# Kernel tuning notes

Hardware: AMD Instinct MI355X
Metric: run time of the kernel (lower is better)

Reference implementation:

```python
import jax, jax.numpy as jnp
import numpy as np

N = 100000   # nodes
E = 1600000  # edges (before self-loops)
HIDDEN = 256
BN_EPS = 1e-5


def setup_inputs() -> dict:
    key = jax.random.key(0)
    ks = jax.random.split(key, 16)
    def lin(k, i, o):
        return jax.random.normal(k, (i, o), jnp.float32) / np.float32(np.sqrt(i))
    inp = {
        "x": jax.random.normal(ks[0], (N, 21), jnp.float32),
        "edge_index": jax.random.randint(ks[1], (2, E), 0, N),
        # GCNConv weights (stored [in, out]) + biases
        "W1": lin(ks[2], 21, HIDDEN), "b1": jnp.zeros((HIDDEN,), jnp.float32),
        "W2": lin(ks[3], HIDDEN, 112), "b2": jnp.zeros((112,), jnp.float32),
        # dense MLP
        "lin2_w": lin(ks[4], 112, 256), "lin2_b": jnp.zeros((256,), jnp.float32),
        "lin3_w": lin(ks[5], 256, 100), "lin3_b": jnp.zeros((100,), jnp.float32),
        "lin4_w": lin(ks[6], 100, 1),   "lin4_b": jnp.zeros((1,), jnp.float32),
        # batchnorm affine params
        "g1": jnp.ones((112,), jnp.float32), "be1": jnp.zeros((112,), jnp.float32),
        "g2": jnp.ones((256,), jnp.float32), "be2": jnp.zeros((256,), jnp.float32),
        "g3": jnp.ones((100,), jnp.float32), "be3": jnp.zeros((100,), jnp.float32),
    }
    return inp


def _gcn_conv(x, W, b, src, dst, n):
    # PyG GCNConv: h = xW; out_i = sum_j norm_ij * h_j (+ bias), sym-normalized w/ self-loops
    h = x @ W                                              # [N, C]
    deg = jax.ops.segment_sum(jnp.ones(src.shape, h.dtype), dst, num_segments=n)
    dinv = jnp.where(deg > 0, jax.lax.rsqrt(deg), 0.0)
    norm = dinv[src] * dinv[dst]                            # [E']
    out = jax.ops.segment_sum(h[src] * norm[:, None], dst, num_segments=n)
    return out + b


def _bn(x, g, b):
    # train-mode batchnorm: biased batch variance
    m = jnp.mean(x, axis=0)
    v = jnp.mean(jnp.square(x - m), axis=0)
    return (x - m) * jax.lax.rsqrt(v + BN_EPS) * g + b


def reference(x, edge_index, W1, b1, W2, b2, lin2_w, lin2_b, lin3_w, lin3_b,
              lin4_w, lin4_b, g1, be1, g2, be2, g3, be3):
    n = x.shape[0]
    loops = jnp.arange(n, dtype=edge_index.dtype)
    src = jnp.concatenate([edge_index[0], loops])
    dst = jnp.concatenate([edge_index[1], loops])
    h = jax.nn.relu(_gcn_conv(x, W1, b1, src, dst, n))
    h = _gcn_conv(h, W2, b2, src, dst, n)
    h = jax.nn.relu(_bn(h, g1, be1))
    # dropout: identity (eval / deterministic)
    h = jax.nn.relu(_bn(h @ lin2_w + lin2_b, g2, be2))
    h = jax.nn.relu(_bn(h @ lin3_w + lin3_b, g3, be3))
    return h @ lin4_w + lin4_b
```

## Files before the change

kernel.cpp:

```cpp
#include <hip/hip_runtime.h>

#define N_NODES 100000
#define N_EDGES 1600000

typedef _Float16 f16x8 __attribute__((ext_vector_type(8)));
typedef _Float16 f16x4 __attribute__((ext_vector_type(4)));
typedef float fx4 __attribute__((ext_vector_type(4)));

#define NREP 16
#define NBUCK 196
#define CHUNK 8192
#define BCAP 12288

__global__ __launch_bounds__(256) void k_bin(const int* __restrict__ ei,
                                             unsigned* __restrict__ binned,
                                             int* __restrict__ gcount) {
  __shared__ unsigned pr[CHUNK];
  __shared__ unsigned srt[CHUNK];
  __shared__ unsigned char bk[CHUNK];
  __shared__ int hist[256], scanb[256], offs[256], bs[256], gb[256];
  const int t = threadIdx.x;
  const int e0 = blockIdx.x * CHUNK;
  const int n = min(CHUNK, N_EDGES - e0);
  hist[t] = 0;
  __syncthreads();
  for (int i = t; i < n; i += 256) {
    int src = ei[e0 + i], dst = ei[N_EDGES + e0 + i];
    int b = dst >> 9;
    pr[i] = ((unsigned)src << 9) | (unsigned)(dst & 511);
    bk[i] = (unsigned char)b;
    atomicAdd(&hist[b], 1);
  }
  __syncthreads();
  int v = hist[t];
  scanb[t] = v;
  __syncthreads();
  for (int off = 1; off < 256; off <<= 1) {
    int a = (t >= off) ? scanb[t - off] : 0;
    __syncthreads();
    scanb[t] += a;
    __syncthreads();
  }
  offs[t] = scanb[t] - v;
  bs[t] = scanb[t] - v;
  __syncthreads();
  for (int i = t; i < n; i += 256) {
    int b = bk[i];
    int p = atomicAdd(&offs[b], 1);
    srt[p] = pr[i];
  }
  if (t < NBUCK && v > 0) gb[t] = atomicAdd(&gcount[t], v);
  __syncthreads();
  int wave = t >> 6, lane = t & 63;
  for (int b = wave; b < NBUCK; b += 4) {
    int c = hist[b];
    if (c == 0) continue;
    int ls = bs[b], base = gb[b];
    unsigned* dstp = binned + (size_t)b * BCAP + base;
    for (int i = lane; i < c; i += 64) dstp[i] = srt[ls + i];
  }
}

__global__ void k_bscan(const int* __restrict__ gcount, int* __restrict__ gbase) {
  __shared__ int s[256];
  int t = threadIdx.x;
  int v = (t < NBUCK) ? gcount[t] : 0;
  s[t] = v;
  __syncthreads();
  for (int off = 1; off < 256; off <<= 1) {
    int a = (t >= off) ? s[t - off] : 0;
    __syncthreads();
    s[t] += a;
    __syncthreads();
  }
  if (t < NBUCK) gbase[t] = s[t] - v;
}

__global__ __launch_bounds__(256) void k_csr(const unsigned* __restrict__ binned,
                                             const int* __restrict__ gcount,
                                             const int* __restrict__ gbase,
                                             int* __restrict__ rowoff,
                                             int* __restrict__ cnt,
                                             float* __restrict__ dinv,
                                             int* __restrict__ csr) {
  __shared__ int hist[512], offs[512], ps[256];
  __shared__ unsigned srt[BCAP];
  const int b = blockIdx.x, t = threadIdx.x;
  const int n = min(gcount[b], BCAP);
  const int gb0 = gbase[b];
  const unsigned* bp = binned + (size_t)b * BCAP;
  hist[t] = 0;
  hist[t + 256] = 0;
  __syncthreads();
  for (int i = t; i < n; i += 256) atomicAdd(&hist[bp[i] & 511], 1);
  __syncthreads();
  int e0v = hist[2 * t], e1v = hist[2 * t + 1];
  ps[t] = e0v + e1v;
  __syncthreads();
  for (int off = 1; off < 256; off <<= 1) {
    int a = (t >= off) ? ps[t - off] : 0;
    __syncthreads();
    ps[t] += a;
    __syncthreads();
  }
  int excl = ps[t] - (e0v + e1v);
  offs[2 * t] = excl;
  offs[2 * t + 1] = excl + e0v;
  __syncthreads();
#pragma unroll
  for (int u = 0; u < 2; ++u) {
    int j = 2 * t + u;
    int nd = (b << 9) + j;
    if (nd < N_NODES) {
      int c = hist[j];
      cnt[nd] = c;
      dinv[nd] = rsqrtf((float)(c + 1));
      rowoff[nd] = gb0 + offs[j];
    }
  }
  __syncthreads();
  for (int i = t; i < n; i += 256) {
    unsigned p = bp[i];
    int d = p & 511;
    int pos = atomicAdd(&offs[d], 1);
    srt[pos] = p >> 9;
  }
  __syncthreads();
  for (int i = t; i < n; i += 256) csr[gb0 + i] = (int)srt[i];
}

__global__ void k_xpad(const float* __restrict__ x, const float* __restrict__ dinv,
                       _Float16* __restrict__ xs) {
  int idx = blockIdx.x * 256 + threadIdx.x;
  if (idx >= N_NODES * 24) return;
  int r = idx / 24, c = idx - r * 24;
  xs[idx] = (_Float16)((c < 21) ? x[r * 21 + c] * dinv[r] : 0.f);
}

__global__ __launch_bounds__(256) void k_aggx(
    const f16x8* __restrict__ xs3, const float* __restrict__ dinv,
    const int* __restrict__ rowoff, const int* __restrict__ cnt,
    const int* __restrict__ csr, float* __restrict__ aggx) {
  int lane = threadIdx.x & 63, wave = threadIdx.x >> 6;
  int j = lane / 3, c = lane - j * 3;
  if (j >= 21) return;
  int i = blockIdx.x * 84 + wave * 21 + j;
  if (i >= N_NODES) return;
  float di = dinv[i];
  int start = rowoff[i], len = cnt[i];
  f16x8 u = xs3[i * 3 + c];
  float a0[8], a1[8], a2[8], a3[8];
#pragma unroll
  for (int t = 0; t < 8; ++t) { a0[t] = (float)u[t]; a1[t] = a2[t] = a3[t] = 0.f; }
  int e = 0;
  for (; e + 3 < len; e += 4) {
    int s0 = csr[start + e], s1 = csr[start + e + 1];
    int s2 = csr[start + e + 2], s3 = csr[start + e + 3];
    f16x8 u0 = xs3[s0 * 3 + c];
    f16x8 u1 = xs3[s1 * 3 + c];
    f16x8 u2 = xs3[s2 * 3 + c];
    f16x8 u3 = xs3[s3 * 3 + c];
#pragma unroll
    for (int t = 0; t < 8; ++t) {
      a0[t] += (float)u0[t]; a1[t] += (float)u1[t];
      a2[t] += (float)u2[t]; a3[t] += (float)u3[t];
    }
  }
  for (; e < len; ++e) {
    int s0 = csr[start + e];
    f16x8 u0 = xs3[s0 * 3 + c];
#pragma unroll
    for (int t = 0; t < 8; ++t) a0[t] += (float)u0[t];
  }
  float4 r0, r1;
  r0.x = di * (a0[0] + a1[0] + a2[0] + a3[0]);
  r0.y = di * (a0[1] + a1[1] + a2[1] + a3[1]);
  r0.z = di * (a0[2] + a1[2] + a2[2] + a3[2]);
  r0.w = di * (a0[3] + a1[3] + a2[3] + a3[3]);
  r1.x = di * (a0[4] + a1[4] + a2[4] + a3[4]);
  r1.y = di * (a0[5] + a1[5] + a2[5] + a3[5]);
  r1.z = di * (a0[6] + a1[6] + a2[6] + a3[6]);
  r1.w = di * (a0[7] + a1[7] + a2[7] + a3[7]);
  *(float4*)(aggx + (size_t)i * 24 + c * 8) = r0;
  *(float4*)(aggx + (size_t)i * 24 + c * 8 + 4) = r1;
}

__global__ __launch_bounds__(256) void k_gemm1(const float4* __restrict__ aggx4,
                                               const float* __restrict__ W1,
                                               const float* __restrict__ b1,
                                               _Float16* __restrict__ h1) {
  __shared__ float As[32][24];
  int t = threadIdx.x;
  int base = blockIdx.x * 32;
  for (int idx = t; idx < 32 * 6; idx += 256) {
    int m = idx / 6, q = idx - m * 6;
    *(float4*)(&As[m][q * 4]) = aggx4[(base + m) * 6 + q];
  }
  float w[21];
#pragma unroll
  for (int k = 0; k < 21; ++k) w[k] = W1[k * 256 + t];
  float bias = b1[t];
  __syncthreads();
  for (int m = 0; m < 32; ++m) {
    float acc = bias;
#pragma unroll
    for (int k = 0; k < 21; ++k) acc = fmaf(As[m][k], w[k], acc);
    h1[(size_t)(base + m) * 256 + t] = (_Float16)fmaxf(acc, 0.f);
  }
}

template <int K, int KPAD, int NOUT, int NR>
__global__ void k_wcvt(const float* __restrict__ W, _Float16* __restrict__ Wh) {
  int idx = blockIdx.x * 256 + threadIdx.x;
  if (idx >= NR * KPAD) return;
  int n = idx / KPAD, k = idx % KPAD;
  float v = (n < NOUT && k < K) ? W[k * NOUT + n] : 0.f;
  Wh[idx] = (_Float16)v;
}

template <int K, int KPAD, int NT, int MT, int WR, int WC, int MINW,
          bool BN, bool STATS, bool F16IN, bool F16OUT, bool SPLIT>
__global__ __launch_bounds__(256, MINW) void k_mgemm(
    const void* __restrict__ Av, const _Float16* __restrict__ Wt,
    const float* __restrict__ bias, const float* __restrict__ bn_a,
    const float* __restrict__ bn_c, const float* __restrict__ rowscale,
    void* __restrict__ Cv, void* __restrict__ Cv2, int NOUTr,
    float* __restrict__ sums, float* __restrict__ sqs) {
  constexpr int BM = WR * MT * 16;
  constexpr int NR = WC * NT * 16;
  constexpr int BKP = 40;
  constexpr int NC = KPAD / 32;
  constexpr int AIT = BM * 4 / 256;
  constexpr int ABYTES = BM * BKP * 2;
  constexpr int BBYTES = NR * BKP * 2;
  __shared__ __align__(16) char smem[ABYTES + BBYTES];
  _Float16* Ah = (_Float16*)smem;
  _Float16* Bh = (_Float16*)(smem + ABYTES);
  const float* A32 = (const float*)Av;
  const _Float16* A16 = (const _Float16*)Av;
  float* C = (float*)Cv;
  _Float16* C16 = (_Float16*)Cv;
  _Float16* C16b = (_Float16*)Cv2;

  const int tid = threadIdx.x;
  const int lane = tid & 63, wave = tid >> 6;
  const int wr = wave % WR, wc = wave / WR;
  const int quad = lane >> 4, ln = lane & 15;
  const int rowbase = blockIdx.x * BM;

  fx4 acc[MT][NT];
#pragma unroll
  for (int mt = 0; mt < MT; ++mt)
#pragma unroll
    for (int j = 0; j < NT; ++j) acc[mt][j] = (fx4){0.f, 0.f, 0.f, 0.f};

  f16x8 pf16[AIT];
  fx4 pf32a[AIT], pf32b[AIT];

  auto loadA = [&](int kc) {
#pragma unroll
    for (int it = 0; it < AIT; ++it) {
      int idx = tid + it * 256;
      int m = idx >> 2, q = idx & 3;
      int gi = rowbase + m;
      int k = kc * 32 + q * 8;
      bool ok = (gi < N_NODES) && (k < K);
      if constexpr (F16IN) {
        f16x8 z;
#pragma unroll
        for (int t = 0; t < 8; ++t) z[t] = (_Float16)0;
        pf16[it] = ok ? *(const f16x8*)(A16 + (size_t)gi * K + k) : z;
      } else {
        if (ok) {
          pf32a[it] = *(const fx4*)(A32 + (size_t)gi * K + k);
          pf32b[it] = *(const fx4*)(A32 + (size_t)gi * K + k + 4);
        } else {
          pf32a[it] = (fx4){0.f, 0.f, 0.f, 0.f};
          pf32b[it] = (fx4){0.f, 0.f, 0.f, 0.f};
        }
      }
    }
  };

  auto writeA = [&](int kc) {
#pragma unroll
    for (int it = 0; it < AIT; ++it) {
      int idx = tid + it * 256;
      int m = idx >> 2, q = idx & 3;
      int k = kc * 32 + q * 8;
      float vv[8];
      if constexpr (F16IN) {
#pragma unroll
        for (int t = 0; t < 8; ++t) vv[t] = (float)pf16[it][t];
      } else {
#pragma unroll
        for (int t = 0; t < 4; ++t) { vv[t] = pf32a[it][t]; vv[t + 4] = pf32b[it][t]; }
      }
      if constexpr (BN) {
        if (k < K) {
          float4 a0 = *(const float4*)(bn_a + k);
          float4 a1 = *(const float4*)(bn_a + k + 4);
          float4 c0 = *(const float4*)(bn_c + k);
          float4 c1 = *(const float4*)(bn_c + k + 4);
          float av[8] = {a0.x, a0.y, a0.z, a0.w, a1.x, a1.y, a1.z, a1.w};
          float cv[8] = {c0.x, c0.y, c0.z, c0.w, c1.x, c1.y, c1.z, c1.w};
#pragma unroll
          for (int t = 0; t < 8; ++t) vv[t] = fmaxf(fmaf(vv[t], av[t], cv[t]), 0.f);
        }
      }
      f16x8 hv;
#pragma unroll
      for (int t = 0; t < 8; ++t) hv[t] = (_Float16)vv[t];
      *(f16x8*)(Ah + m * BKP + q * 8) = hv;
    }
  };

  loadA(0);
  for (int kc = 0; kc < NC; ++kc) {
    __syncthreads();
    writeA(kc);
    for (int idx = tid; idx < NR * 4; idx += 256) {
      int n = idx >> 2, p = idx & 3;
      *(f16x8*)(Bh + n * BKP + p * 8) =
          *(const f16x8*)(Wt + n * KPAD + kc * 32 + p * 8);
    }
    __syncthreads();
    if (kc + 1 < NC) loadA(kc + 1);
    f16x8 nf[MT];
#pragma unroll
    for (int mt = 0; mt < MT; ++mt) {
      int r = (wr * MT + mt) * 16 + ln;
      nf[mt] = *(const f16x8*)(Ah + r * BKP + quad * 8);
    }
#pragma unroll
    for (int j = 0; j < NT; ++j) {
      int n = (wc * NT + j) * 16 + ln;
      f16x8 wh = *(const f16x8*)(Bh + n * BKP + quad * 8);
#pragma unroll
      for (int mt = 0; mt < MT; ++mt)
        acc[mt][j] = __builtin_amdgcn_mfma_f32_16x16x32_f16(wh, nf[mt], acc[mt][j], 0, 0, 0);
    }
  }

  float* s_s = (float*)smem;
  float* s_q = s_s + NR;
  __syncthreads();
  if constexpr (STATS) {
    for (int c = tid; c < 2 * NR; c += 256) s_s[c] = 0.f;
    __syncthreads();
  }
  float rs[MT];
#pragma unroll
  for (int mt = 0; mt < MT; ++mt) {
    int nd = rowbase + (wr * MT + mt) * 16 + ln;
    rs[mt] = (rowscale != nullptr && nd < N_NODES) ? rowscale[nd] : 1.f;
  }
#pragma unroll
  for (int j = 0; j < NT; ++j) {
    int ch0 = (wc * NT + j) * 16 + quad * 4;
    bool cv = ch0 < NOUTr;
    float4 b4 = make_float4(0.f, 0.f, 0.f, 0.f);
    if (cv && bias != nullptr) b4 = *(const float4*)(bias + ch0);
    float sc[4] = {0.f, 0.f, 0.f, 0.f}, sq[4] = {0.f, 0.f, 0.f, 0.f};
#pragma unroll
    for (int mt = 0; mt < MT; ++mt) {
      int nd = rowbase + (wr * MT + mt) * 16 + ln;
      if (nd < N_NODES && cv) {
        float v0 = (acc[mt][j][0] + b4.x) * rs[mt];
        float v1 = (acc[mt][j][1] + b4.y) * rs[mt];
        float v2 = (acc[mt][j][2] + b4.z) * rs[mt];
        float v3 = (acc[mt][j][3] + b4.w) * rs[mt];
        if constexpr (F16OUT) {
          f16x4 o = {(_Float16)v0, (_Float16)v1, (_Float16)v2, (_Float16)v3};
          if constexpr (SPLIT) {
            _Float16* dp = (ch0 < 56)
                ? C16 + (size_t)nd * 64 + ch0
                : C16b + (size_t)nd * 64 + (ch0 - 56);
            *(f16x4*)dp = o;
          } else {
            *(f16x4*)(C16 + (size_t)nd * NOUTr + ch0) = o;
          }
        } else {
          float4 o = make_float4(v0, v1, v2, v3);
          *(float4*)(C + (size_t)nd * NOUTr + ch0) = o;
        }
        if constexpr (STATS) {
          sc[0] += v0; sq[0] = fmaf(v0, v0, sq[0]);
          sc[1] += v1; sq[1] = fmaf(v1, v1, sq[1]);
          sc[2] += v2; sq[2] = fmaf(v2, v2, sq[2]);
          sc[3] += v3; sq[3] = fmaf(v3, v3, sq[3]);
        }
      }
    }
    if constexpr (STATS) {
      if (cv) {
#pragma unroll
        for (int r = 0; r < 4; ++r) {
          float s = sc[r], q = sq[r];
          s += __shfl_xor(s, 1); q += __shfl_xor(q, 1);
          s += __shfl_xor(s, 2); q += __shfl_xor(q, 2);
          s += __shfl_xor(s, 4); q += __shfl_xor(q, 4);
          s += __shfl_xor(s, 8); q += __shfl_xor(q, 8);
          if (ln == 0) {
            atomicAdd(&s_s[ch0 + r], s);
            atomicAdd(&s_q[ch0 + r], q);
          }
        }
      }
    }
  }
  if constexpr (STATS) {
    __syncthreads();
    int rep = (blockIdx.x & (NREP - 1));
    for (int c = tid; c < NR; c += 256) {
      if (c < NOUTr) {
        atomicAdd(&sums[rep * NOUTr + c], s_s[c]);
        atomicAdd(&sqs[rep * NOUTr + c], s_q[c]);
      }
    }
  }
}

__global__ __launch_bounds__(256) void k_agg2(
    const f16x8* __restrict__ t2x8, const float* __restrict__ dinv,
    const int* __restrict__ rowoff, const int* __restrict__ cnt,
    const int* __restrict__ csr, const float* __restrict__ b2,
    _Float16* __restrict__ g2, int off) {
  int lane = threadIdx.x & 63, wave = threadIdx.x >> 6;
  int j = lane >> 3, c = lane & 7;
  int i = blockIdx.x * 32 + wave * 8 + j;
  float di = dinv[i];
  int start = rowoff[i], len = cnt[i];
  f16x8 u = t2x8[i * 8 + c];
  float a0[8], a1[8], a2[8], a3[8];
#pragma unroll
  for (int t = 0; t < 8; ++t) { a0[t] = (float)u[t]; a1[t] = a2[t] = a3[t] = 0.f; }
  int e = 0;
  for (; e + 3 < len; e += 4) {
    int s0 = csr[start + e], s1 = csr[start + e + 1];
    int s2 = csr[start + e + 2], s3 = csr[start + e + 3];
    f16x8 u0 = t2x8[s0 * 8 + c];
    f16x8 u1 = t2x8[s1 * 8 + c];
    f16x8 u2 = t2x8[s2 * 8 + c];
    f16x8 u3 = t2x8[s3 * 8 + c];
#pragma unroll
    for (int t = 0; t < 8; ++t) {
      a0[t] += (float)u0[t]; a1[t] += (float)u1[t];
      a2[t] += (float)u2[t]; a3[t] += (float)u3[t];
    }
  }
  for (; e < len; ++e) {
    int s0 = csr[start + e];
    f16x8 u0 = t2x8[s0 * 8 + c];
#pragma unroll
    for (int t = 0; t < 8; ++t) a0[t] += (float)u0[t];
  }
  if (c < 7) {
    float4 blo = *(const float4*)(b2 + off + c * 8);
    float4 bhi = *(const float4*)(b2 + off + c * 8 + 4);
    float bb[8] = {blo.x, blo.y, blo.z, blo.w, bhi.x, bhi.y, bhi.z, bhi.w};
    f16x8 o;
#pragma unroll
    for (int t = 0; t < 8; ++t)
      o[t] = (_Float16)fmaf(di, a0[t] + a1[t] + a2[t] + a3[t], bb[t]);
    *(f16x8*)(g2 + (size_t)i * 112 + off + c * 8) = o;
  }
}

template <int C>
__global__ void k_colstats16(const _Float16* __restrict__ X, float* __restrict__ sums,
                             float* __restrict__ sqs) {
  int c = threadIdx.x;
  if (c >= C) return;
  int chunk = (N_NODES + gridDim.x - 1) / gridDim.x;
  int i0 = blockIdx.x * chunk;
  int i1 = min(N_NODES, i0 + chunk);
  float s = 0.f, q = 0.f;
  for (int i = i0; i < i1; ++i) {
    float v = (float)X[(size_t)i * C + c];
    s += v;
    q = fmaf(v, v, q);
  }
  int rep = (blockIdx.x & (NREP - 1));
  atomicAdd(&sums[rep * C + c], s);
  atomicAdd(&sqs[rep * C + c], q);
}

template <int C>
__global__ void k_bnfinal(const float* __restrict__ sums, const float* __restrict__ sqs,
                          const float* __restrict__ gamma, const float* __restrict__ beta,
                          float* __restrict__ bn_a, float* __restrict__ bn_c) {
  int c = threadIdx.x;
  if (c >= C) return;
  float s = 0.f, q = 0.f;
#pragma unroll
  for (int r = 0; r < NREP; ++r) {
    s += sums[r * C + c];
    q += sqs[r * C + c];
  }
  const float inv_n = 1.0f / (float)N_NODES;
  float mean = s * inv_n;
  float var = fmaxf(q * inv_n - mean * mean, 0.f);
  float rstd = 1.0f / sqrtf(var + 1e-5f);
  float a = gamma[c] * rstd;
  bn_a[c] = a;
  bn_c[c] = beta[c] - mean * a;
}

__global__ void k_final(const float* __restrict__ h4, const float* __restrict__ bn_a,
                        const float* __restrict__ bn_c, const float* __restrict__ w4,
                        const float* __restrict__ b4, float* __restrict__ out) {
  int lane = threadIdx.x & 63;
  int i = blockIdx.x * 4 + (threadIdx.x >> 6);
  float acc = fmaxf(fmaf(h4[(size_t)i * 100 + lane], bn_a[lane], bn_c[lane]), 0.f) * w4[lane];
  if (lane < 36) {
    int k = lane + 64;
    acc += fmaxf(fmaf(h4[(size_t)i * 100 + k], bn_a[k], bn_c[k]), 0.f) * w4[k];
  }
#pragma unroll
  for (int off = 32; off >= 1; off >>= 1) acc += __shfl_down(acc, off);
  if (lane == 0) out[i] = acc + b4[0];
}

extern "C" void kernel_launch(void* const* d_in, const int* in_sizes, int n_in,
                              void* d_out, int out_size, void* d_ws, size_t ws_size,
                              hipStream_t stream) {
  const float* x   = (const float*)d_in[0];
  const int*   ei  = (const int*)d_in[1];
  const float* W1  = (const float*)d_in[2];
  const float* b1  = (const float*)d_in[3];
  const float* W2  = (const float*)d_in[4];
  const float* b2  = (const float*)d_in[5];
  const float* l2w = (const float*)d_in[6];
  const float* l2b = (const float*)d_in[7];
  const float* l3w = (const float*)d_in[8];
  const float* l3b = (const float*)d_in[9];
  const float* l4w = (const float*)d_in[10];
  const float* l4b = (const float*)d_in[11];
  const float* g1  = (const float*)d_in[12];
  const float* be1 = (const float*)d_in[13];
  const float* g2w = (const float*)d_in[14];
  const float* be2 = (const float*)d_in[15];
  const float* g3  = (const float*)d_in[16];
  const float* be3 = (const float*)d_in[17];
  float* out = (float*)d_out;

  char* base = (char*)d_ws;
  size_t off = 0;
  auto alloc = [&](size_t bytes) -> char* {
    char* p = base + off;
    off = (off + bytes + 255) & ~(size_t)255;
    return p;
  };
  int*   cnt    = (int*)alloc((size_t)N_NODES * 4);
  int*   rowoff = (int*)alloc((size_t)N_NODES * 4);
  float* dinv   = (float*)alloc((size_t)N_NODES * 4);
  int*   csr    = (int*)alloc((size_t)N_EDGES * 4);
  unsigned* binned = (unsigned*)alloc((size_t)NBUCK * BCAP * 4);
  int*   gcount = (int*)alloc(NBUCK * 4);
  int*   gbase  = (int*)alloc(NBUCK * 4);
  float* stats  = (float*)alloc((size_t)NREP * 960 * 4);
  float* bnco   = (float*)alloc(960 * 4);
  _Float16* xs  = (_Float16*)alloc((size_t)N_NODES * 24 * 2);
  float* aggx   = (float*)alloc((size_t)N_NODES * 24 * 4);
  _Float16* h1  = (_Float16*)alloc((size_t)N_NODES * 256 * 2);
  _Float16* t2a = (_Float16*)alloc((size_t)N_NODES * 64 * 2);
  _Float16* t2b = (_Float16*)alloc((size_t)N_NODES * 64 * 2);
  _Float16* g2h = (_Float16*)alloc((size_t)N_NODES * 112 * 2);
  float* h4     = (float*)alloc((size_t)N_NODES * 112 * 4);
  _Float16* wt2 = (_Float16*)alloc(112 * 256 * 2);
  _Float16* wt3 = (_Float16*)alloc(256 * 128 * 2);
  _Float16* wt4 = (_Float16*)alloc(112 * 256 * 2);

  float* sums1 = stats;
  float* sqs1  = sums1 + NREP * 112;
  float* sums2 = sqs1 + NREP * 112;
  float* sqs2  = sums2 + NREP * 256;
  float* sums3 = sqs2 + NREP * 256;
  float* sqs3  = sums3 + NREP * 112;
  float* bn_a1 = bnco + 0,   *bn_c1 = bnco + 112;
  float* bn_a2 = bnco + 224, *bn_c2 = bnco + 480;
  float* bn_a3 = bnco + 736, *bn_c3 = bnco + 848;

  hipMemsetAsync(gcount, 0, NBUCK * 4, stream);
  hipMemsetAsync(stats, 0, (size_t)NREP * 960 * 4, stream);

  k_bin<<<NBUCK, 256, 0, stream>>>(ei, binned, gcount);
  k_bscan<<<1, 256, 0, stream>>>(gcount, gbase);
  k_csr<<<NBUCK, 256, 0, stream>>>(binned, gcount, gbase, rowoff, cnt, dinv, csr);

  k_wcvt<256, 256, 112, 112><<<112, 256, 0, stream>>>(W2, wt2);
  k_wcvt<112, 128, 256, 256><<<128, 256, 0, stream>>>(l2w, wt3);
  k_wcvt<256, 256, 100, 112><<<112, 256, 0, stream>>>(l3w, wt4);

  k_xpad<<<(N_NODES * 24 + 255) / 256, 256, 0, stream>>>(x, dinv, xs);
  k_aggx<<<(N_NODES + 83) / 84, 256, 0, stream>>>((const f16x8*)xs, dinv, rowoff,
                                                  cnt, csr, aggx);
  k_gemm1<<<3125, 256, 0, stream>>>((const float4*)aggx, W1, b1, h1);

  k_mgemm<256, 256, 7, 2, 4, 1, 4, false, false, true, true, true>
      <<<782, 256, 0, stream>>>(h1, wt2, nullptr, nullptr, nullptr, dinv,
                                t2a, t2b, 112, nullptr, nullptr);
  k_agg2<<<3125, 256, 0, stream>>>((const f16x8*)t2a, dinv, rowoff, cnt, csr, b2,
                                   g2h, 0);
  k_agg2<<<3125, 256, 0, stream>>>((const f16x8*)t2b, dinv, rowoff, cnt, csr, b2,
                                   g2h, 56);

  k_colstats16<112><<<1600, 128, 0, stream>>>(g2h, sums1, sqs1);
  k_bnfinal<112><<<1, 128, 0, stream>>>(sums1, sqs1, g1, be1, bn_a1, bn_c1);

  k_mgemm<112, 128, 8, 2, 2, 2, 4, true, true, true, true, false>
      <<<1563, 256, 0, stream>>>(g2h, wt3, l2b, bn_a1, bn_c1, nullptr,
                                 h1, nullptr, 256, sums2, sqs2);
  k_bnfinal<256><<<1, 256, 0, stream>>>(sums2, sqs2, g2w, be2, bn_a2, bn_c2);

  k_mgemm<256, 256, 7, 2, 4, 1, 4, true, true, true, false, false>
      <<<782, 256, 0, stream>>>(h1, wt4, l3b, bn_a2, bn_c2, nullptr,
                                h4, nullptr, 100, sums3, sqs3);
  k_bnfinal<100><<<1, 128, 0, stream>>>(sums3, sqs3, g3, be3, bn_a3, bn_c3);

  k_final<<<25000, 256, 0, stream>>>(h4, bn_a3, bn_c3, l4w, l4b, out);
}
```

Baseline: 411.4 us.

## Restructure dense GEMM to preload full weight tile and load A directly to registers

The MFMA GEMM kernel now loads the whole weight tile (all K) into shared memory once and has each wave read its A fragments directly from global memory into registers. This removes the per-K-chunk A staging through LDS and the two barriers per iteration. The 256-wide GEMM is split across a second grid dimension over output channels, and the lin3 output buffer h4 is stored as fp16 instead of fp32 to halve its write and read traffic. The trade-off is that A loads are no longer software-prefetched, the B tile uses more shared memory, occupancy hints change, and h4 loses precision.

```diff
diff --git a/kernel.cpp b/kernel.cpp
--- a/kernel.cpp
+++ b/kernel.cpp
@@ -218,153 +218,103 @@
   Wh[idx] = (_Float16)v;
 }
 
-template <int K, int KPAD, int NT, int MT, int WR, int WC, int MINW,
-          bool BN, bool STATS, bool F16IN, bool F16OUT, bool SPLIT>
+template <int K, int KPAD, int NT, int MT, int MINW,
+          bool BN, bool STATS, bool F16OUT, bool SPLIT>
 __global__ __launch_bounds__(256, MINW) void k_mgemm(
-    const void* __restrict__ Av, const _Float16* __restrict__ Wt,
+    const _Float16* __restrict__ A16, const _Float16* __restrict__ Wt,
     const float* __restrict__ bias, const float* __restrict__ bn_a,
     const float* __restrict__ bn_c, const float* __restrict__ rowscale,
     void* __restrict__ Cv, void* __restrict__ Cv2, int NOUTr,
     float* __restrict__ sums, float* __restrict__ sqs) {
+  constexpr int WR = 4;
   constexpr int BM = WR * MT * 16;
-  constexpr int NR = WC * NT * 16;
-  constexpr int BKP = 40;
+  constexpr int NR = NT * 16;
+  constexpr int KPS = KPAD + 8;
   constexpr int NC = KPAD / 32;
-  constexpr int AIT = BM * 4 / 256;
-  constexpr int ABYTES = BM * BKP * 2;
-  constexpr int BBYTES = NR * BKP * 2;
-  __shared__ __align__(16) char smem[ABYTES + BBYTES];
-  _Float16* Ah = (_Float16*)smem;
-  _Float16* Bh = (_Float16*)(smem + ABYTES);
-  const float* A32 = (const float*)Av;
-  const _Float16* A16 = (const _Float16*)Av;
+  __shared__ __align__(16) _Float16 Bh[NR * KPS];
+
+  const int tid = threadIdx.x;
+  const int lane = tid & 63, wave = tid >> 6;
+  const int quad = lane >> 4, ln = lane & 15;
+  const int rowbase = blockIdx.x * BM;
+  const int chbase = blockIdx.y * NR;
+
+  for (int idx = tid; idx < NR * (KPAD / 8); idx += 256) {
+    int n = idx / (KPAD / 8), p = idx % (KPAD / 8);
+    *(f16x8*)(Bh + n * KPS + p * 8) =
+        *(const f16x8*)(Wt + (size_t)(chbase + n) * KPAD + p * 8);
+  }
+  __syncthreads();
+
+  fx4 acc[MT][NT];
+#pragma unroll
+  for (int mt = 0; mt < MT; ++mt)
+#pragma unroll
+    for (int j = 0; j < NT; ++j) acc[mt][j] = (fx4){0.f, 0.f, 0.f, 0.f};
+
+  for (int kc = 0; kc < NC; ++kc) {
+    const int k0 = kc * 32 + quad * 8;
+    f16x8 af[MT];
+#pragma unroll
+    for (int mt = 0; mt < MT; ++mt) {
+      int gi = rowbase + (wave * MT + mt) * 16 + ln;
+      bool ok = (gi < N_NODES) && (k0 < K);
+      f16x8 z;
+#pragma unroll
+      for (int t = 0; t < 8; ++t) z[t] = (_Float16)0;
+      af[mt] = ok ? *(const f16x8*)(A16 + (size_t)gi * K + k0) : z;
+    }
+    if constexpr (BN) {
+      if (k0 < K) {
+        float4 ba0 = *(const float4*)(bn_a + k0);
+        float4 ba1 = *(const float4*)(bn_a + k0 + 4);
+        float4 bc0 = *(const float4*)(bn_c + k0);
+        float4 bc1 = *(const float4*)(bn_c + k0 + 4);
+        float av[8] = {ba0.x, ba0.y, ba0.z, ba0.w, ba1.x, ba1.y, ba1.z, ba1.w};
+        float cv[8] = {bc0.x, bc0.y, bc0.z, bc0.w, bc1.x, bc1.y, bc1.z, bc1.w};
+#pragma unroll
+        for (int mt = 0; mt < MT; ++mt)
+#pragma unroll
+          for (int t = 0; t < 8; ++t)
+            af[mt][t] = (_Float16)fmaxf(fmaf((float)af[mt][t], av[t], cv[t]), 0.f);
+      }
+    }
+#pragma unroll
+    for (int j = 0; j < NT; ++j) {
+      f16x8 wh = *(const f16x8*)(Bh + (j * 16 + ln) * KPS + kc * 32 + quad * 8);
+#pragma unroll
+      for (int mt = 0; mt < MT; ++mt)
+        acc[mt][j] = __builtin_amdgcn_mfma_f32_16x16x32_f16(wh, af[mt], acc[mt][j], 0, 0, 0);
+    }
+  }
+
+  float* s_s = (float*)Bh;
+  float* s_q = s_s + NR;
+  __syncthreads();
+  if constexpr (STATS) {
+    for (int c = tid; c < 2 * NR; c += 256) s_s[c] = 0.f;
+    __syncthreads();
+  }
+  float rs[MT];
+#pragma unroll
+  for (int mt = 0; mt < MT; ++mt) {
+    int nd = rowbase + (wave * MT + mt) * 16 + ln;
+    rs[mt] = (rowscale != nullptr && nd < N_NODES) ? rowscale[nd] : 1.f;
+  }
   float* C = (float*)Cv;
   _Float16* C16 = (_Float16*)Cv;
   _Float16* C16b = (_Float16*)Cv2;
-
-  const int tid = threadIdx.x;
-  const int lane = tid & 63, wave = tid >> 6;
-  const int wr = wave % WR, wc = wave / WR;
-  const int quad = lane >> 4, ln = lane & 15;
-  const int rowbase = blockIdx.x * BM;
-
-  fx4 acc[MT][NT];
-#pragma unroll
-  for (int mt = 0; mt < MT; ++mt)
-#pragma unroll
-    for (int j = 0; j < NT; ++j) acc[mt][j] = (fx4){0.f, 0.f, 0.f, 0.f};
-
-  f16x8 pf16[AIT];
-  fx4 pf32a[AIT], pf32b[AIT];
-
-  auto loadA = [&](int kc) {
-#pragma unroll
-    for (int it = 0; it < AIT; ++it) {
-      int idx = tid + it * 256;
-      int m = idx >> 2, q = idx & 3;
-      int gi = rowbase + m;
-      int k = kc * 32 + q * 8;
-      bool ok = (gi < N_NODES) && (k < K);
-      if constexpr (F16IN) {
-        f16x8 z;
-#pragma unroll
-        for (int t = 0; t < 8; ++t) z[t] = (_Float16)0;
-        pf16[it] = ok ? *(const f16x8*)(A16 + (size_t)gi * K + k) : z;
-      } else {
-        if (ok) {
-          pf32a[it] = *(const fx4*)(A32 + (size_t)gi * K + k);
-          pf32b[it] = *(const fx4*)(A32 + (size_t)gi * K + k + 4);
-        } else {
-          pf32a[it] = (fx4){0.f, 0.f, 0.f, 0.f};
-          pf32b[it] = (fx4){0.f, 0.f, 0.f, 0.f};
-        }
-      }
-    }
-  };
-
-  auto writeA = [&](int kc) {
-#pragma unroll
-    for (int it = 0; it < AIT; ++it) {
-      int idx = tid + it * 256;
-      int m = idx >> 2, q = idx & 3;
-      int k = kc * 32 + q * 8;
-      float vv[8];
-      if constexpr (F16IN) {
-#pragma unroll
-        for (int t = 0; t < 8; ++t) vv[t] = (float)pf16[it][t];
-      } else {
-#pragma unroll
-        for (int t = 0; t < 4; ++t) { vv[t] = pf32a[it][t]; vv[t + 4] = pf32b[it][t]; }
-      }
-      if constexpr (BN) {
-        if (k < K) {
-          float4 a0 = *(const float4*)(bn_a + k);
-          float4 a1 = *(const float4*)(bn_a + k + 4);
-          float4 c0 = *(const float4*)(bn_c + k);
-          float4 c1 = *(const float4*)(bn_c + k + 4);
-          float av[8] = {a0.x, a0.y, a0.z, a0.w, a1.x, a1.y, a1.z, a1.w};
-          float cv[8] = {c0.x, c0.y, c0.z, c0.w, c1.x, c1.y, c1.z, c1.w};
-#pragma unroll
-          for (int t = 0; t < 8; ++t) vv[t] = fmaxf(fmaf(vv[t], av[t], cv[t]), 0.f);
-        }
-      }
-      f16x8 hv;
-#pragma unroll
-      for (int t = 0; t < 8; ++t) hv[t] = (_Float16)vv[t];
-      *(f16x8*)(Ah + m * BKP + q * 8) = hv;
-    }
-  };
-
-  loadA(0);
-  for (int kc = 0; kc < NC; ++kc) {
-    __syncthreads();
-    writeA(kc);
-    for (int idx = tid; idx < NR * 4; idx += 256) {
-      int n = idx >> 2, p = idx & 3;
-      *(f16x8*)(Bh + n * BKP + p * 8) =
-          *(const f16x8*)(Wt + n * KPAD + kc * 32 + p * 8);
-    }
-    __syncthreads();
-    if (kc + 1 < NC) loadA(kc + 1);
-    f16x8 nf[MT];
-#pragma unroll
-    for (int mt = 0; mt < MT; ++mt) {
-      int r = (wr * MT + mt) * 16 + ln;
-      nf[mt] = *(const f16x8*)(Ah + r * BKP + quad * 8);
-    }
-#pragma unroll
-    for (int j = 0; j < NT; ++j) {
-      int n = (wc * NT + j) * 16 + ln;
-      f16x8 wh = *(const f16x8*)(Bh + n * BKP + quad * 8);
-#pragma unroll
-      for (int mt = 0; mt < MT; ++mt)
-        acc[mt][j] = __builtin_amdgcn_mfma_f32_16x16x32_f16(wh, nf[mt], acc[mt][j], 0, 0, 0);
-    }
-  }
-
-  float* s_s = (float*)smem;
-  float* s_q = s_s + NR;
-  __syncthreads();
-  if constexpr (STATS) {
-    for (int c = tid; c < 2 * NR; c += 256) s_s[c] = 0.f;
-    __syncthreads();
-  }
-  float rs[MT];
-#pragma unroll
-  for (int mt = 0; mt < MT; ++mt) {
-    int nd = rowbase + (wr * MT + mt) * 16 + ln;
-    rs[mt] = (rowscale != nullptr && nd < N_NODES) ? rowscale[nd] : 1.f;
-  }
 #pragma unroll
   for (int j = 0; j < NT; ++j) {
-    int ch0 = (wc * NT + j) * 16 + quad * 4;
+    int lch = j * 16 + quad * 4;
+    int ch0 = chbase + lch;
     bool cv = ch0 < NOUTr;
     float4 b4 = make_float4(0.f, 0.f, 0.f, 0.f);
     if (cv && bias != nullptr) b4 = *(const float4*)(bias + ch0);
     float sc[4] = {0.f, 0.f, 0.f, 0.f}, sq[4] = {0.f, 0.f, 0.f, 0.f};
 #pragma unroll
     for (int mt = 0; mt < MT; ++mt) {
-      int nd = rowbase + (wr * MT + mt) * 16 + ln;
+      int nd = rowbase + (wave * MT + mt) * 16 + ln;
       if (nd < N_NODES && cv) {
         float v0 = (acc[mt][j][0] + b4.x) * rs[mt];
         float v1 = (acc[mt][j][1] + b4.y) * rs[mt];
@@ -402,8 +352,8 @@
           s += __shfl_xor(s, 4); q += __shfl_xor(q, 4);
           s += __shfl_xor(s, 8); q += __shfl_xor(q, 8);
           if (ln == 0) {
-            atomicAdd(&s_s[ch0 + r], s);
-            atomicAdd(&s_q[ch0 + r], q);
+            atomicAdd(&s_s[lch + r], s);
+            atomicAdd(&s_q[lch + r], q);
           }
         }
       }
@@ -413,9 +363,10 @@
     __syncthreads();
     int rep = (blockIdx.x & (NREP - 1));
     for (int c = tid; c < NR; c += 256) {
-      if (c < NOUTr) {
-        atomicAdd(&sums[rep * NOUTr + c], s_s[c]);
-        atomicAdd(&sqs[rep * NOUTr + c], s_q[c]);
+      int gc = chbase + c;
+      if (gc < NOUTr) {
+        atomicAdd(&sums[rep * NOUTr + gc], s_s[c]);
+        atomicAdd(&sqs[rep * NOUTr + gc], s_q[c]);
       }
     }
   }
@@ -507,15 +458,15 @@
   bn_c[c] = beta[c] - mean * a;
 }
 
-__global__ void k_final(const float* __restrict__ h4, const float* __restrict__ bn_a,
+__global__ void k_final(const _Float16* __restrict__ h4, const float* __restrict__ bn_a,
                         const float* __restrict__ bn_c, const float* __restrict__ w4,
                         const float* __restrict__ b4, float* __restrict__ out) {
   int lane = threadIdx.x & 63;
   int i = blockIdx.x * 4 + (threadIdx.x >> 6);
-  float acc = fmaxf(fmaf(h4[(size_t)i * 100 + lane], bn_a[lane], bn_c[lane]), 0.f) * w4[lane];
+  float acc = fmaxf(fmaf((float)h4[(size_t)i * 100 + lane], bn_a[lane], bn_c[lane]), 0.f) * w4[lane];
   if (lane < 36) {
     int k = lane + 64;
-    acc += fmaxf(fmaf(h4[(size_t)i * 100 + k], bn_a[k], bn_c[k]), 0.f) * w4[k];
+    acc += fmaxf(fmaf((float)h4[(size_t)i * 100 + k], bn_a[k], bn_c[k]), 0.f) * w4[k];
   }
 #pragma unroll
   for (int off = 32; off >= 1; off >>= 1) acc += __shfl_down(acc, off);
@@ -567,7 +518,7 @@
   _Float16* t2a = (_Float16*)alloc((size_t)N_NODES * 64 * 2);
   _Float16* t2b = (_Float16*)alloc((size_t)N_NODES * 64 * 2);
   _Float16* g2h = (_Float16*)alloc((size_t)N_NODES * 112 * 2);
-  float* h4     = (float*)alloc((size_t)N_NODES * 112 * 4);
+  _Float16* h4  = (_Float16*)alloc((size_t)N_NODES * 112 * 2);
   _Float16* wt2 = (_Float16*)alloc(112 * 256 * 2);
   _Float16* wt3 = (_Float16*)alloc(256 * 128 * 2);
   _Float16* wt4 = (_Float16*)alloc(112 * 256 * 2);
@@ -598,9 +549,9 @@
                                                   cnt, csr, aggx);
   k_gemm1<<<3125, 256, 0, stream>>>((const float4*)aggx, W1, b1, h1);
 
-  k_mgemm<256, 256, 7, 2, 4, 1, 4, false, false, true, true, true>
-      <<<782, 256, 0, stream>>>(h1, wt2, nullptr, nullptr, nullptr, dinv,
-                                t2a, t2b, 112, nullptr, nullptr);
+  k_mgemm<256, 256, 7, 2, 2, false, false, true, true>
+      <<<dim3(782, 1), 256, 0, stream>>>(h1, wt2, nullptr, nullptr, nullptr, dinv,
+                                         t2a, t2b, 112, nullptr, nullptr);
   k_agg2<<<3125, 256, 0, stream>>>((const f16x8*)t2a, dinv, rowoff, cnt, csr, b2,
                                    g2h, 0);
   k_agg2<<<3125, 256, 0, stream>>>((const f16x8*)t2b, dinv, rowoff, cnt, csr, b2,
@@ -609,14 +560,14 @@
   k_colstats16<112><<<1600, 128, 0, stream>>>(g2h, sums1, sqs1);
   k_bnfinal<112><<<1, 128, 0, stream>>>(sums1, sqs1, g1, be1, bn_a1, bn_c1);
 
-  k_mgemm<112, 128, 8, 2, 2, 2, 4, true, true, true, true, false>
-      <<<1563, 256, 0, stream>>>(g2h, wt3, l2b, bn_a1, bn_c1, nullptr,
-                                 h1, nullptr, 256, sums2, sqs2);
+  k_mgemm<112, 128, 8, 2, 3, true, true, true, false>
+      <<<dim3(782, 2), 256, 0, stream>>>(g2h, wt3, l2b, bn_a1, bn_c1, nullptr,
+                                         h1, nullptr, 256, sums2, sqs2);
   k_bnfinal<256><<<1, 256, 0, stream>>>(sums2, sqs2, g2w, be2, bn_a2, bn_c2);
 
-  k_mgemm<256, 256, 7, 2, 4, 1, 4, true, true, true, false, false>
-      <<<782, 256, 0, stream>>>(h1, wt4, l3b, bn_a2, bn_c2, nullptr,
-                                h4, nullptr, 100, sums3, sqs3);
+  k_mgemm<256, 256, 7, 2, 2, true, true, true, false>
+      <<<dim3(782, 1), 256, 0, stream>>>(h1, wt4, l3b, bn_a2, bn_c2, nullptr,
+                                         h4, nullptr, 100, sums3, sqs3);
   k_bnfinal<100><<<1, 128, 0, stream>>>(sums3, sqs3, g3, be3, bn_a3, bn_c3);
 
   k_final<<<25000, 256, 0, stream>>>(h4, bn_a3, bn_c3, l4w, l4b, out);
```

After: 427.6 us. 3.9% more time.

## Add register-direct A MFMA GEMM with resident weights; store lin3 output in fp16

Applied to the files above, without the earlier changes.

Adds k_mgemm2, which keeps the full weight slice for a block resident in shared memory and loads A fragments straight from global into registers. The BN+ReLU is applied in registers and the A tile is no longer staged through LDS. The grid is split over output channels (782x2), and the kernel is used for the lin2 layer. The lin3 output h4 is now written as fp16 instead of fp32, which halves that intermediate's traffic into k_final at some cost in precision. Dead F16IN template paths are removed from k_mgemm.

```diff
diff --git a/kernel.cpp b/kernel.cpp
--- a/kernel.cpp
+++ b/kernel.cpp
@@ -219,9 +219,9 @@
 }
 
 template <int K, int KPAD, int NT, int MT, int WR, int WC, int MINW,
-          bool BN, bool STATS, bool F16IN, bool F16OUT, bool SPLIT>
+          bool BN, bool STATS, bool F16OUT, bool SPLIT>
 __global__ __launch_bounds__(256, MINW) void k_mgemm(
-    const void* __restrict__ Av, const _Float16* __restrict__ Wt,
+    const _Float16* __restrict__ A16, const _Float16* __restrict__ Wt,
     const float* __restrict__ bias, const float* __restrict__ bn_a,
     const float* __restrict__ bn_c, const float* __restrict__ rowscale,
     void* __restrict__ Cv, void* __restrict__ Cv2, int NOUTr,
@@ -236,8 +236,6 @@
   __shared__ __align__(16) char smem[ABYTES + BBYTES];
   _Float16* Ah = (_Float16*)smem;
   _Float16* Bh = (_Float16*)(smem + ABYTES);
-  const float* A32 = (const float*)Av;
-  const _Float16* A16 = (const _Float16*)Av;
   float* C = (float*)Cv;
   _Float16* C16 = (_Float16*)Cv;
   _Float16* C16b = (_Float16*)Cv2;
@@ -255,7 +253,6 @@
     for (int j = 0; j < NT; ++j) acc[mt][j] = (fx4){0.f, 0.f, 0.f, 0.f};
 
   f16x8 pf16[AIT];
-  fx4 pf32a[AIT], pf32b[AIT];
 
   auto loadA = [&](int kc) {
 #pragma unroll
@@ -265,20 +262,10 @@
       int gi = rowbase + m;
       int k = kc * 32 + q * 8;
       bool ok = (gi < N_NODES) && (k < K);
-      if constexpr (F16IN) {
-        f16x8 z;
-#pragma unroll
-        for (int t = 0; t < 8; ++t) z[t] = (_Float16)0;
-        pf16[it] = ok ? *(const f16x8*)(A16 + (size_t)gi * K + k) : z;
-      } else {
-        if (ok) {
-          pf32a[it] = *(const fx4*)(A32 + (size_t)gi * K + k);
-          pf32b[it] = *(const fx4*)(A32 + (size_t)gi * K + k + 4);
-        } else {
-          pf32a[it] = (fx4){0.f, 0.f, 0.f, 0.f};
-          pf32b[it] = (fx4){0.f, 0.f, 0.f, 0.f};
-        }
-      }
+      f16x8 z;
+#pragma unroll
+      for (int t = 0; t < 8; ++t) z[t] = (_Float16)0;
+      pf16[it] = ok ? *(const f16x8*)(A16 + (size_t)gi * K + k) : z;
     }
   };
 
@@ -289,13 +276,8 @@
       int m = idx >> 2, q = idx & 3;
       int k = kc * 32 + q * 8;
       float vv[8];
-      if constexpr (F16IN) {
-#pragma unroll
-        for (int t = 0; t < 8; ++t) vv[t] = (float)pf16[it][t];
-      } else {
-#pragma unroll
-        for (int t = 0; t < 4; ++t) { vv[t] = pf32a[it][t]; vv[t + 4] = pf32b[it][t]; }
-      }
+#pragma unroll
+      for (int t = 0; t < 8; ++t) vv[t] = (float)pf16[it][t];
       if constexpr (BN) {
         if (k < K) {
           float4 a0 = *(const float4*)(bn_a + k);
@@ -421,6 +403,152 @@
   }
 }
 
+template <int K, int KPAD, int NT, int MT, int MINW,
+          bool BN, bool STATS, bool F16OUT>
+__global__ __launch_bounds__(256, MINW) void k_mgemm2(
+    const _Float16* __restrict__ A16, const _Float16* __restrict__ Wt,
+    const float* __restrict__ bias, const float* __restrict__ bn_a,
+    const float* __restrict__ bn_c, const float* __restrict__ rowscale,
+    void* __restrict__ Cv, int NOUTr, float* __restrict__ sums,
+    float* __restrict__ sqs) {
+  constexpr int WR = 4;
+  constexpr int BM = WR * MT * 16;
+  constexpr int NR = NT * 16;
+  constexpr int KPS = KPAD + 8;
+  constexpr int NC = KPAD / 32;
+  __shared__ __align__(16) _Float16 Bh[NR * KPS];
+
+  const int tid = threadIdx.x;
+  const int lane = tid & 63, wave = tid >> 6;
+  const int quad = lane >> 4, ln = lane & 15;
+  const int rowbase = blockIdx.x * BM;
+  const int chbase = blockIdx.y * NR;
+
+  for (int idx = tid; idx < NR * (KPAD / 8); idx += 256) {
+    int n = idx / (KPAD / 8), p = idx % (KPAD / 8);
+    *(f16x8*)(Bh + n * KPS + p * 8) =
+        *(const f16x8*)(Wt + (size_t)(chbase + n) * KPAD + p * 8);
+  }
+  __syncthreads();
+
+  fx4 acc[MT][NT];
+#pragma unroll
+  for (int mt = 0; mt < MT; ++mt)
+#pragma unroll
+    for (int j = 0; j < NT; ++j) acc[mt][j] = (fx4){0.f, 0.f, 0.f, 0.f};
+
+  for (int kc = 0; kc < NC; ++kc) {
+    const int k0 = kc * 32 + quad * 8;
+    f16x8 af[MT];
+#pragma unroll
+    for (int mt = 0; mt < MT; ++mt) {
+      int gi = rowbase + (wave * MT + mt) * 16 + ln;
+      bool ok = (gi < N_NODES) && (k0 < K);
+      f16x8 z;
+#pragma unroll
+      for (int t = 0; t < 8; ++t) z[t] = (_Float16)0;
+      af[mt] = ok ? *(const f16x8*)(A16 + (size_t)gi * K + k0) : z;
+    }
+    if constexpr (BN) {
+      if (k0 < K) {
+        float4 ba0 = *(const float4*)(bn_a + k0);
+        float4 ba1 = *(const float4*)(bn_a + k0 + 4);
+        float4 bc0 = *(const float4*)(bn_c + k0);
+        float4 bc1 = *(const float4*)(bn_c + k0 + 4);
+        float av[8] = {ba0.x, ba0.y, ba0.z, ba0.w, ba1.x, ba1.y, ba1.z, ba1.w};
+        float cv[8] = {bc0.x, bc0.y, bc0.z, bc0.w, bc1.x, bc1.y, bc1.z, bc1.w};
+#pragma unroll
+        for (int mt = 0; mt < MT; ++mt)
+#pragma unroll
+          for (int t = 0; t < 8; ++t)
+            af[mt][t] = (_Float16)fmaxf(fmaf((float)af[mt][t], av[t], cv[t]), 0.f);
+      }
+    }
+#pragma unroll
+    for (int j = 0; j < NT; ++j) {
+      f16x8 wh = *(const f16x8*)(Bh + (j * 16 + ln) * KPS + kc * 32 + quad * 8);
+#pragma unroll
+      for (int mt = 0; mt < MT; ++mt)
+        acc[mt][j] = __builtin_amdgcn_mfma_f32_16x16x32_f16(wh, af[mt], acc[mt][j], 0, 0, 0);
+    }
+  }
+
+  float* s_s = (float*)Bh;
+  float* s_q = s_s + NR;
+  __syncthreads();
+  if constexpr (STATS) {
+    for (int c = tid; c < 2 * NR; c += 256) s_s[c] = 0.f;
+    __syncthreads();
+  }
+  float rs[MT];
+#pragma unroll
+  for (int mt = 0; mt < MT; ++mt) {
+    int nd = rowbase + (wave * MT + mt) * 16 + ln;
+    rs[mt] = (rowscale != nullptr && nd < N_NODES) ? rowscale[nd] : 1.f;
+  }
+  float* C = (float*)Cv;
+  _Float16* C16 = (_Float16*)Cv;
+#pragma unroll
+  for (int j = 0; j < NT; ++j) {
+    int lch = j * 16 + quad * 4;
+    int ch0 = chbase + lch;
+    bool cv = ch0 < NOUTr;
+    float4 b4 = make_float4(0.f, 0.f, 0.f, 0.f);
+    if (cv && bias != nullptr) b4 = *(const float4*)(bias + ch0);
+    float sc[4] = {0.f, 0.f, 0.f, 0.f}, sq[4] = {0.f, 0.f, 0.f, 0.f};
+#pragma unroll
+    for (int mt = 0; mt < MT; ++mt) {
+      int nd = rowbase + (wave * MT + mt) * 16 + ln;
+      if (nd < N_NODES && cv) {
+        float v0 = (acc[mt][j][0] + b4.x) * rs[mt];
+        float v1 = (acc[mt][j][1] + b4.y) * rs[mt];
+        float v2 = (acc[mt][j][2] + b4.z) * rs[mt];
+        float v3 = (acc[mt][j][3] + b4.w) * rs[mt];
+        if constexpr (F16OUT) {
+          f16x4 o = {(_Float16)v0, (_Float16)v1, (_Float16)v2, (_Float16)v3};
+          *(f16x4*)(C16 + (size_t)nd * NOUTr + ch0) = o;
+        } else {
+          float4 o = make_float4(v0, v1, v2, v3);
+          *(float4*)(C + (size_t)nd * NOUTr + ch0) = o;
+        }
+        if constexpr (STATS) {
+          sc[0] += v0; sq[0] = fmaf(v0, v0, sq[0]);
+          sc[1] += v1; sq[1] = fmaf(v1, v1, sq[1]);
+          sc[2] += v2; sq[2] = fmaf(v2, v2, sq[2]);
+          sc[3] += v3; sq[3] = fmaf(v3, v3, sq[3]);
+        }
+      }
+    }
+    if constexpr (STATS) {
+      if (cv) {
+#pragma unroll
+        for (int r = 0; r < 4; ++r) {
+          float s = sc[r], q = sq[r];
+          s += __shfl_xor(s, 1); q += __shfl_xor(q, 1);
+          s += __shfl_xor(s, 2); q += __shfl_xor(q, 2);
+          s += __shfl_xor(s, 4); q += __shfl_xor(q, 4);
+          s += __shfl_xor(s, 8); q += __shfl_xor(q, 8);
+          if (ln == 0) {
+            atomicAdd(&s_s[lch + r], s);
+            atomicAdd(&s_q[lch + r], q);
+          }
+        }
+      }
+    }
+  }
+  if constexpr (STATS) {
+    __syncthreads();
+    int rep = (blockIdx.x & (NREP - 1));
+    for (int c = tid; c < NR; c += 256) {
+      int gc = chbase + c;
+      if (gc < NOUTr) {
+        atomicAdd(&sums[rep * NOUTr + gc], s_s[c]);
+        atomicAdd(&sqs[rep * NOUTr + gc], s_q[c]);
+      }
+    }
+  }
+}
+
 __global__ __launch_bounds__(256) void k_agg2(
     const f16x8* __restrict__ t2x8, const float* __restrict__ dinv,
     const int* __restrict__ rowoff, const int* __restrict__ cnt,
@@ -507,15 +635,15 @@
   bn_c[c] = beta[c] - mean * a;
 }
 
-__global__ void k_final(const float* __restrict__ h4, const float* __restrict__ bn_a,
+__global__ void k_final(const _Float16* __restrict__ h4, const float* __restrict__ bn_a,
                         const float* __restrict__ bn_c, const float* __restrict__ w4,
                         const float* __restrict__ b4, float* __restrict__ out) {
   int lane = threadIdx.x & 63;
   int i = blockIdx.x * 4 + (threadIdx.x >> 6);
-  float acc = fmaxf(fmaf(h4[(size_t)i * 100 + lane], bn_a[lane], bn_c[lane]), 0.f) * w4[lane];
+  float acc = fmaxf(fmaf((float)h4[(size_t)i * 100 + lane], bn_a[lane], bn_c[lane]), 0.f) * w4[lane];
   if (lane < 36) {
     int k = lane + 64;
-    acc += fmaxf(fmaf(h4[(size_t)i * 100 + k], bn_a[k], bn_c[k]), 0.f) * w4[k];
+    acc += fmaxf(fmaf((float)h4[(size_t)i * 100 + k], bn_a[k], bn_c[k]), 0.f) * w4[k];
   }
 #pragma unroll
   for (int off = 32; off >= 1; off >>= 1) acc += __shfl_down(acc, off);
@@ -567,7 +695,7 @@
   _Float16* t2a = (_Float16*)alloc((size_t)N_NODES * 64 * 2);
   _Float16* t2b = (_Float16*)alloc((size_t)N_NODES * 64 * 2);
   _Float16* g2h = (_Float16*)alloc((size_t)N_NODES * 112 * 2);
-  float* h4     = (float*)alloc((size_t)N_NODES * 112 * 4);
+  _Float16* h4  = (_Float16*)alloc((size_t)N_NODES * 112 * 2);
   _Float16* wt2 = (_Float16*)alloc(112 * 256 * 2);
   _Float16* wt3 = (_Float16*)alloc(256 * 128 * 2);
   _Float16* wt4 = (_Float16*)alloc(112 * 256 * 2);
@@ -598,7 +726,7 @@
                                                   cnt, csr, aggx);
   k_gemm1<<<3125, 256, 0, stream>>>((const float4*)aggx, W1, b1, h1);
 
-  k_mgemm<256, 256, 7, 2, 4, 1, 4, false, false, true, true, true>
+  k_mgemm<256, 256, 7, 2, 4, 1, 4, false, false, true, true>
       <<<782, 256, 0, stream>>>(h1, wt2, nullptr, nullptr, nullptr, dinv,
                                 t2a, t2b, 112, nullptr, nullptr);
   k_agg2<<<3125, 256, 0, stream>>>((const f16x8*)t2a, dinv, rowoff, cnt, csr, b2,
@@ -609,12 +737,12 @@
   k_colstats16<112><<<1600, 128, 0, stream>>>(g2h, sums1, sqs1);
   k_bnfinal<112><<<1, 128, 0, stream>>>(sums1, sqs1, g1, be1, bn_a1, bn_c1);
 
-  k_mgemm<112, 128, 8, 2, 2, 2, 4, true, true, true, true, false>
-      <<<1563, 256, 0, stream>>>(g2h, wt3, l2b, bn_a1, bn_c1, nullptr,
-                                 h1, nullptr, 256, sums2, sqs2);
+  k_mgemm2<112, 128, 8, 2, 3, true, true, true>
+      <<<dim3(782, 2), 256, 0, stream>>>(g2h, wt3, l2b, bn_a1, bn_c1, nullptr,
+                                         h1, 256, sums2, sqs2);
   k_bnfinal<256><<<1, 256, 0, stream>>>(sums2, sqs2, g2w, be2, bn_a2, bn_c2);
 
-  k_mgemm<256, 256, 7, 2, 4, 1, 4, true, true, true, false, false>
+  k_mgemm<256, 256, 7, 2, 4, 1, 4, true, true, true, false>
       <<<782, 256, 0, stream>>>(h1, wt4, l3b, bn_a2, bn_c2, nullptr,
                                 h4, nullptr, 100, sums3, sqs3);
   k_bnfinal<100><<<1, 128, 0, stream>>>(sums3, sqs3, g3, be3, bn_a3, bn_c3);
```

After: 410.6 us (median of 2 runs). No clear change (-0.2%).
